# Optimization experiments

Measured on AMD Instinct MI355X. Metric: run time of the kernel, lower is better.

## Reference

```python
import jax, jax.numpy as jnp
import numpy as np

B, S, E, H = 2, 2048, 1024, 16
D = E // H  # head_dim = 64


def setup_inputs() -> dict:
    key = jax.random.key(0)
    ks = jax.random.split(key, 12)
    sc = 1.0 / np.sqrt(E)
    inp = {
        "query": jax.random.normal(ks[0], (B, S, E), jnp.float32),
        "key": jax.random.normal(ks[1], (B, S, E), jnp.float32),
        "value": jax.random.normal(ks[2], (B, S, E), jnp.float32),
        # causal mask: 1 where attending is allowed, 0 where blocked
        "mask": jnp.tril(jnp.ones((S, S), jnp.int32))[None, None, :, :],
        "Wq": jax.random.normal(ks[3], (E, E), jnp.float32) * sc,
        "bq": jax.random.normal(ks[4], (E,), jnp.float32) * sc,
        "Wk": jax.random.normal(ks[5], (E, E), jnp.float32) * sc,
        "bk": jax.random.normal(ks[6], (E,), jnp.float32) * sc,
        "Wv": jax.random.normal(ks[7], (E, E), jnp.float32) * sc,
        "bv": jax.random.normal(ks[8], (E,), jnp.float32) * sc,
        "Wo": jax.random.normal(ks[9], (E, E), jnp.float32) * sc,
        "bo": jax.random.normal(ks[10], (E,), jnp.float32) * sc,
    }
    return inp


def reference(query, key, value, mask, Wq, bq, Wk, bk, Wv, bv, Wo, bo):
    scale = jnp.asarray(np.sqrt(D), query.dtype)
    # Linear projections (torch Linear: x @ W.T + b)
    Q = query @ Wq.T + bq
    K = key @ Wk.T + bk
    V = value @ Wv.T + bv
    # [B, S, E] -> [B, H, S, D]
    Q = Q.reshape(B, -1, H, D).transpose(0, 2, 1, 3)
    K = K.reshape(B, -1, H, D).transpose(0, 2, 1, 3)
    V = V.reshape(B, -1, H, D).transpose(0, 2, 1, 3)
    # full [B, H, Sq, Sk] score matrix, as in the source
    scores = jnp.einsum("bhqd,bhkd->bhqk", Q, K) / scale
    scores = jnp.where(mask == 0, jnp.asarray(-1e10, scores.dtype), scores)
    weights = jax.nn.softmax(scores, axis=-1)
    weighted = jnp.einsum("bhqk,bhkd->bhqd", weights, V)
    concat = weighted.transpose(0, 2, 1, 3).reshape(B, -1, E)
    return concat @ Wo.T + bo
```

## Files before the change

### kernel.cpp

```cpp
#include <hip/hip_runtime.h>
#include <math.h>

#define BB 2
#define SS 2048
#define EE 1024
#define HH 16
#define DD 64

typedef unsigned short u16;
typedef __attribute__((ext_vector_type(8))) short short8;
typedef __attribute__((ext_vector_type(4))) float f32x4;

__device__ __forceinline__ u16 f2bf(float x) {
    union { float f; unsigned u; } v; v.f = x;
    return (u16)((v.u + 0x7fffu + ((v.u >> 16) & 1u)) >> 16);
}

__device__ __forceinline__ float exp2_fast(float x) {
    float r;
    asm("v_exp_f32 %0, %1" : "=v"(r) : "v"(x));
    return r;
}

#define GLL16(gp, lp) \
    __builtin_amdgcn_global_load_lds( \
        (const __attribute__((address_space(1))) void*)(gp), \
        (__attribute__((address_space(3))) void*)(lp), 16, 0, 0)

#define BARRIER do { asm volatile("" ::: "memory"); \
                     __builtin_amdgcn_s_barrier();  \
                     asm volatile("" ::: "memory"); } while (0)
#define VMW4 asm volatile("s_waitcnt vmcnt(4)" ::: "memory")
#define VMW0 asm volatile("s_waitcnt vmcnt(0)" ::: "memory")
#define LG0  asm volatile("s_waitcnt lgkmcnt(0)" ::: "memory")
#define SCHED0 __builtin_amdgcn_sched_barrier(0)

#define QSCALE 0.18033688f

__global__ __launch_bounds__(256)
void cvt_bf16(const float* __restrict__ s0, const float* __restrict__ s1,
              const float* __restrict__ s2, const float* __restrict__ s3,
              u16* __restrict__ d0, u16* __restrict__ d1,
              u16* __restrict__ d2, u16* __restrict__ d3)
{
    const int z = blockIdx.y;
    const float* s; u16* d;
    switch (z) {
        case 0: s = s0; d = d0; break;
        case 1: s = s1; d = d1; break;
        case 2: s = s2; d = d2; break;
        default: s = s3; d = d3; break;
    }
    const int i = (blockIdx.x * 256 + threadIdx.x) * 8;
    float4 a = *(const float4*)(s + i);
    float4 b = *(const float4*)(s + i + 4);
    short8 r;
    r[0] = (short)f2bf(a.x); r[1] = (short)f2bf(a.y);
    r[2] = (short)f2bf(a.z); r[3] = (short)f2bf(a.w);
    r[4] = (short)f2bf(b.x); r[5] = (short)f2bf(b.y);
    r[6] = (short)f2bf(b.z); r[7] = (short)f2bf(b.w);
    *(short8*)(d + i) = r;
}

__global__ __launch_bounds__(256, 3)
void gemm_qkv(const float* __restrict__ Xq, const float* __restrict__ Xk,
              const float* __restrict__ Xv,
              const u16* __restrict__ Wqb, const u16* __restrict__ Wkb,
              const u16* __restrict__ Wvb,
              const float* __restrict__ bq, const float* __restrict__ bk,
              const float* __restrict__ bv,
              u16* __restrict__ Qh, u16* __restrict__ Kh, u16* __restrict__ Vth)
{
    __shared__ __align__(16) u16 LS[2][2][128][32];
#define LA (LS[0])
#define LB (LS[1])

    const int bid = blockIdx.x;
    const int swz = (bid & 7) * 96 + (bid >> 3);
    const int z   = swz >> 8;
    const int rem = swz & 255;
    const int m0  = (rem >> 3) * 128;
    const int n0  = (rem & 7) * 128;

    const float* X = (z == 0) ? Xq : (z == 1) ? Xk : Xv;
    const u16* Wt = (z == 0) ? Wqb : (z == 1) ? Wkb : Wvb;
    const float* bias = (z == 0) ? bq : (z == 1) ? bk : bv;
    u16* out = (z == 0) ? Qh : (z == 1) ? Kh : Vth;

    const int t = threadIdx.x;
    const int w = t >> 6, l = t & 63;
    const int ln = l & 15, hi = l >> 4;
    const int wr = w >> 1, wc = w & 1;

    const int ar = t >> 1, ah = t & 1;
    const float* Xrow = X + (size_t)(m0 + ar) * 1024 + ah * 16;
    const int fa   = (ar >> 1) & 3;
    const int gpa0 = (2 * ah)     ^ fa;
    const int gpa1 = (2 * ah + 1) ^ fa;

    const int brow = t >> 2, gp4 = t & 3;
    const int gl4  = gp4 ^ (brow & 3);
    const u16* Wp0 = Wt + (size_t)(n0 + brow) * 1024 + gl4 * 8;
    const u16* Wp1 = Wt + (size_t)(n0 + 64 + brow) * 1024 + gl4 * 8;

    f32x4 acc[4][4];
    #pragma unroll
    for (int i = 0; i < 4; i++)
        #pragma unroll
        for (int j = 0; j < 4; j++)
            acc[i][j] = (f32x4){0.f, 0.f, 0.f, 0.f};

    float4 e0, e1, e2, e3;
    float4 o0, o1, o2, o3;

#define ISSUE_B(buf, k0_) {                                                  \
        GLL16(Wp0 + (k0_), &LB[buf][brow][gp4 * 8]);                         \
        GLL16(Wp1 + (k0_), &LB[buf][brow + 64][gp4 * 8]);                    \
    }
#define LOAD_A(S0, S1, S2, S3, k0_) {                                        \
        S0 = *(const float4*)(Xrow + (k0_));                                 \
        S1 = *(const float4*)(Xrow + (k0_) + 4);                             \
        S2 = *(const float4*)(Xrow + (k0_) + 8);                             \
        S3 = *(const float4*)(Xrow + (k0_) + 12);                            \
    }
#define CVT_A(buf, S0, S1, S2, S3) {                                         \
        uint4 u0, u1;                                                        \
        u0.x = f2bf(S0.x) | ((unsigned)f2bf(S0.y) << 16);                    \
        u0.y = f2bf(S0.z) | ((unsigned)f2bf(S0.w) << 16);                    \
        u0.z = f2bf(S1.x) | ((unsigned)f2bf(S1.y) << 16);                    \
        u0.w = f2bf(S1.z) | ((unsigned)f2bf(S1.w) << 16);                    \
        u1.x = f2bf(S2.x) | ((unsigned)f2bf(S2.y) << 16);                    \
        u1.y = f2bf(S2.z) | ((unsigned)f2bf(S2.w) << 16);                    \
        u1.z = f2bf(S3.x) | ((unsigned)f2bf(S3.y) << 16);                    \
        u1.w = f2bf(S3.z) | ((unsigned)f2bf(S3.w) << 16);                    \
        *(uint4*)&LA[buf][ar][gpa0 * 8] = u0;                                \
        *(uint4*)&LA[buf][ar][gpa1 * 8] = u1;                                \
    }
#define COMPUTE(la_, lb_) {                                                  \
        _Pragma("unroll")                                                    \
        for (int mi = 0; mi < 4; mi++)                                       \
            af[mi] = *(const short8*)&LA[la_][wr*64 + mi*16 + ln]            \
                         [(hi ^ ((ln >> 1) & 3)) * 8];                       \
        _Pragma("unroll")                                                    \
        for (int nj = 0; nj < 4; nj++)                                       \
            bf[nj] = *(const short8*)&LB[lb_][wc*64 + nj*16 + ln]            \
                         [(hi ^ (ln & 3)) * 8];                              \
        _Pragma("unroll")                                                    \
        for (int mi = 0; mi < 4; mi++)                                       \
            _Pragma("unroll")                                                \
            for (int nj = 0; nj < 4; nj++)                                   \
                acc[mi][nj] = __builtin_amdgcn_mfma_f32_16x16x32_bf16(       \
                    af[mi], bf[nj], acc[mi][nj], 0, 0, 0);                   \
    }

    short8 af[4], bf[4];

    LOAD_A(e0, e1, e2, e3, 0);
    CVT_A(0, e0, e1, e2, e3);
    ISSUE_B(0, 0); SCHED0;
    LOAD_A(o0, o1, o2, o3, 32); SCHED0;
    VMW4;
    LG0; BARRIER;

    for (int it = 0; it < 15; ++it) {
        const int k0 = it * 64;
        ISSUE_B(1, k0 + 32); SCHED0;
        LOAD_A(e0, e1, e2, e3, k0 + 64); SCHED0;
        COMPUTE(0, 0);
        CVT_A(1, o0, o1, o2, o3);
        VMW4;
        LG0; BARRIER;
        ISSUE_B(0, k0 + 64); SCHED0;
        LOAD_A(o0, o1, o2, o3, k0 + 96); SCHED0;
        COMPUTE(1, 1);
        CVT_A(0, e0, e1, e2, e3);
        VMW4;
        LG0; BARRIER;
    }
    ISSUE_B(1, 992); SCHED0;
    COMPUTE(0, 0);
    CVT_A(1, o0, o1, o2, o3);
    VMW0;
    LG0; BARRIER;
    COMPUTE(1, 1);
#undef ISSUE_B
#undef LOAD_A
#undef CVT_A
#undef COMPUTE

    u16* T = &LS[0][0][0][0];
    const int b = m0 >> 11;

    if (z == 2) {
        #pragma unroll
        for (int mi = 0; mi < 4; mi++) {
            #pragma unroll
            for (int nj = 0; nj < 4; nj++) {
                const int nc = wc * 64 + nj * 16 + ln;
                const float bv2 = bias[n0 + nc];
                const int sr0 = wr * 64 + mi * 16 + hi * 4;
                uint2 pk;
                pk.x = f2bf(acc[mi][nj][0] + bv2)
                     | ((unsigned)f2bf(acc[mi][nj][1] + bv2) << 16);
                pk.y = f2bf(acc[mi][nj][2] + bv2)
                     | ((unsigned)f2bf(acc[mi][nj][3] + bv2) << 16);
                const int gp = (sr0 >> 2) ^ (nc & 31);
                *(uint2*)&T[nc * 128 + gp * 4] = pk;
            }
        }
        __syncthreads();
        const int s0 = m0 & 2047;
        const int sidx = t & 15;
        const int ncr0 = t >> 4;
        #pragma unroll
        for (int i = 0; i < 8; i++) {
            const int nc = ncr0 + i * 16;
            const int a  = sidx * 2;
            const int pa = a ^ (nc & 31);
            const int pb = (a + 1) ^ (nc & 31);
            uint2 lo  = *(const uint2*)&T[nc * 128 + pa * 4];
            uint2 hi2 = *(const uint2*)&T[nc * 128 + pb * 4];
            uint4 vd = make_uint4(lo.x, lo.y, hi2.x, hi2.y);
            const int h = (n0 >> 6) + (nc >> 6);
            const int d = nc & 63;
            *(uint4*)&out[(((size_t)(b * HH + h) * 64 + d) << 11) + s0 + sidx * 8] = vd;
        }
    } else {
        #pragma unroll
        for (int mi = 0; mi < 4; mi++) {
            #pragma unroll
            for (int nj = 0; nj < 4; nj++) {
                const int nb = n0 + wc * 64 + nj * 16 + ln;
                const float bv2 = bias[nb];
                const int h = nb >> 6, d = nb & 63;
                #pragma unroll
                for (int r = 0; r < 4; r++) {
                    const int m = m0 + wr * 64 + mi * 16 + hi * 4 + r;
                    float v = acc[mi][nj][r] + bv2;
                    if (z == 0) v *= QSCALE;
                    const int s = m & 2047;
                    out[((((size_t)(b * HH + h)) << 11) + s) * 64 + d] = f2bf(v);
                }
            }
        }
    }
#undef LA
#undef LB
}

__global__ __launch_bounds__(256)
void gemm_out(const u16* __restrict__ Xb, const u16* __restrict__ Wb,
              const float* __restrict__ bias, float* __restrict__ outp)
{
    __shared__ __align__(16) u16 As[2][64][32];
    __shared__ __align__(16) u16 Bs[2][128][32];

    const int bid = blockIdx.x;
    const int swz = (bid & 7) * 64 + (bid >> 3);
    const int m0  = (swz >> 3) * 64;
    const int n0  = (swz & 7) * 128;

    const int t = threadIdx.x;
    const int w = t >> 6, l = t & 63;
    const int ln = l & 15, hi = l >> 4;
    const int wr = w >> 1, wc = w & 1;

    const int row0 = t >> 2, gp4 = t & 3;
    const int gl4  = gp4 ^ (row0 & 3);

    f32x4 acc[2][4];
    #pragma unroll
    for (int i = 0; i < 2; i++)
        #pragma unroll
        for (int j = 0; j < 4; j++)
            acc[i][j] = (f32x4){0.f, 0.f, 0.f, 0.f};

#define OSTAGE(buf, k0_) { \
    GLL16(Xb + (size_t)(m0 + row0) * 1024 + (k0_) + gl4 * 8,        \
          &As[buf][row0][gp4 * 8]);                                  \
    GLL16(Wb + (size_t)(n0 + row0) * 1024 + (k0_) + gl4 * 8,        \
          &Bs[buf][row0][gp4 * 8]);                                  \
    GLL16(Wb + (size_t)(n0 + 64 + row0) * 1024 + (k0_) + gl4 * 8,   \
          &Bs[buf][row0 + 64][gp4 * 8]); }

    OSTAGE(0, 0);
    __syncthreads();
    int cur = 0;
    for (int k0 = 0; k0 < 1024; k0 += 32) {
        if (k0 + 32 < 1024) OSTAGE(cur ^ 1, k0 + 32);
        short8 af[2], bfr[4];
        #pragma unroll
        for (int mi = 0; mi < 2; mi++)
            af[mi] = *(const short8*)&As[cur][wr*32 + mi*16 + ln][(hi ^ (ln & 3))*8];
        #pragma unroll
        for (int nj = 0; nj < 4; nj++)
            bfr[nj] = *(const short8*)&Bs[cur][wc*64 + nj*16 + ln][(hi ^ (ln & 3))*8];
        #pragma unroll
        for (int mi = 0; mi < 2; mi++)
            #pragma unroll
            for (int nj = 0; nj < 4; nj++)
                acc[mi][nj] = __builtin_amdgcn_mfma_f32_16x16x32_bf16(
                    af[mi], bfr[nj], acc[mi][nj], 0, 0, 0);
        __syncthreads();
        cur ^= 1;
    }
#undef OSTAGE

    #pragma unroll
    for (int mi = 0; mi < 2; mi++) {
        #pragma unroll
        for (int nj = 0; nj < 4; nj++) {
            const int nb = n0 + wc * 64 + nj * 16 + ln;
            const float bv2 = bias[nb];
            #pragma unroll
            for (int r = 0; r < 4; r++) {
                const int m = m0 + wr * 32 + mi * 16 + hi * 4 + r;
                outp[(size_t)m * 1024 + nb] = acc[mi][nj][r] + bv2;
            }
        }
    }
}

__global__ __launch_bounds__(256)
void attn_mfma(const u16* __restrict__ Qh, const u16* __restrict__ Kh,
               const u16* __restrict__ Vt, u16* __restrict__ Cc)
{
    __shared__ __align__(16) u16 Ks[2][2][4][64][8];
    __shared__ __align__(16) u16 Vs[2][2][4][64][8];
    __shared__ __align__(16) u16 Ps[4][16][64];
    const int bh = blockIdx.x;
    const int y  = 31 - blockIdx.y;
    const int q0 = y * 64;
    const int t = threadIdx.x, w = t >> 6, l = t & 63;
    const int ln = l & 15, hi = l >> 4;
    const size_t base = (size_t)bh * SS * DD;
    const int qg = q0 + w * 16 + ln;

    short8 qf0, qf1;
    {
        const u16* qp = Qh + base + (size_t)qg * 64 + hi * 8;
        qf0 = *(const short8*)qp;
        qf1 = *(const short8*)(qp + 32);
    }
    f32x4 o[4];
    #pragma unroll
    for (int dj = 0; dj < 4; dj++) o[dj] = (f32x4){0.f, 0.f, 0.f, 0.f};
    float mrun = -INFINITY, lrun = 0.f;

#define STAGE(buf, key0_)                                                        \
    {                                                                            \
        _Pragma("unroll")                                                        \
        for (int i_ = 0; i_ < 4; i_++) {                                         \
            const int id_ = w + i_ * 4;                                          \
            if (id_ < 8) {                                                       \
                const int dc_ = id_ >> 2, kg_ = id_ & 3;                         \
                const u16* gp_ = Kh + base + (size_t)((key0_) + l) * 64          \
                                 + dc_ * 32 + kg_ * 8;                           \
                GLL16(gp_, &Ks[buf][dc_][kg_][0][0]);                            \
            } else {                                                             \
                const int kc_ = (id_ >> 2) & 1, kg_ = id_ & 3;                   \
                const u16* gp_ = Vt + base + (size_t)l * SS + (key0_)            \
                                 + kc_ * 32 + kg_ * 8;                           \
                GLL16(gp_, &Vs[buf][kc_][kg_][0][0]);                            \
            }                                                                    \
        }                                                                        \
    }

    STAGE(0, 0);
    __syncthreads();
    int cur = 0;
    const int nkt = y + 1;
    for (int kt = 0; kt < nkt; kt++) {
        const int key0 = kt * 64;
        if (kt + 1 < nkt) STAGE(cur ^ 1, key0 + 64);

        f32x4 st[4];
        __builtin_amdgcn_s_setprio(1);
        #pragma unroll
        for (int kt4 = 0; kt4 < 4; kt4++) {
            short8 ka = *(const short8*)&Ks[cur][0][hi][kt4 * 16 + ln][0];
            short8 kb = *(const short8*)&Ks[cur][1][hi][kt4 * 16 + ln][0];
            f32x4 zz = (f32x4){0.f, 0.f, 0.f, 0.f};
            zz = __builtin_amdgcn_mfma_f32_16x16x32_bf16(ka, qf0, zz, 0, 0, 0);
            zz = __builtin_amdgcn_mfma_f32_16x16x32_bf16(kb, qf1, zz, 0, 0, 0);
            st[kt4] = zz;
        }
        __builtin_amdgcn_s_setprio(0);
        if (kt == y) {
            #pragma unroll
            for (int kt4 = 0; kt4 < 4; kt4++)
                #pragma unroll
                for (int r = 0; r < 4; r++)
                    if (key0 + kt4 * 16 + hi * 4 + r > qg)
                        st[kt4][r] = -INFINITY;
        }

        float tmax = -INFINITY;
        #pragma unroll
        for (int kt4 = 0; kt4 < 4; kt4++)
            #pragma unroll
            for (int r = 0; r < 4; r++)
                tmax = fmaxf(tmax, st[kt4][r]);
        tmax = fmaxf(tmax, __shfl_xor(tmax, 16));
        tmax = fmaxf(tmax, __shfl_xor(tmax, 32));
        if (__ballot(tmax > mrun + 8.f)) {
            const float mnew = fmaxf(mrun, tmax);
            const float alpha = exp2_fast(mrun - mnew);
            lrun *= alpha;
            mrun = mnew;
            #pragma unroll
            for (int r = 0; r < 4; r++) {
                const float ar = __shfl(alpha, hi * 4 + r);
                #pragma unroll
                for (int dj = 0; dj < 4; dj++) o[dj][r] *= ar;
            }
        }
        float p[4][4];
        float lsum = 0.f;
        #pragma unroll
        for (int kt4 = 0; kt4 < 4; kt4++)
            #pragma unroll
            for (int r = 0; r < 4; r++) {
                p[kt4][r] = exp2_fast(st[kt4][r] - mrun);
                lsum += p[kt4][r];
            }
        lsum += __shfl_xor(lsum, 16);
        lsum += __shfl_xor(lsum, 32);
        lrun += lsum;

        char* prow = ((char*)Ps) + (w * 16 + ln) * 128 + (hi & 1) * 8;
        #pragma unroll
        for (int kt4 = 0; kt4 < 4; kt4++) {
            unsigned dw0, dw1;
            asm("v_cvt_pk_bf16_f32 %0, %1, %2" : "=v"(dw0)
                : "v"(p[kt4][0]), "v"(p[kt4][1]));
            asm("v_cvt_pk_bf16_f32 %0, %1, %2" : "=v"(dw1)
                : "v"(p[kt4][2]), "v"(p[kt4][3]));
            const int g = (2 * kt4 + (hi >> 1)) ^ (ln & 7);
            *(uint2*)(prow + g * 16) = make_uint2(dw0, dw1);
        }

        __builtin_amdgcn_s_setprio(1);
        #pragma unroll
        for (int kc = 0; kc < 2; kc++) {
            const int gr = (kc * 4 + hi) ^ (ln & 7);
            short8 pa = *(const short8*)(((char*)Ps) + (w * 16 + ln) * 128 + gr * 16);
            #pragma unroll
            for (int dj = 0; dj < 4; dj++) {
                short8 vb = *(const short8*)&Vs[cur][kc][hi][dj * 16 + ln][0];
                o[dj] = __builtin_amdgcn_mfma_f32_16x16x32_bf16(pa, vb, o[dj], 0, 0, 0);
            }
        }
        __builtin_amdgcn_s_setprio(0);
        __syncthreads();
        cur ^= 1;
    }
#undef STAGE

    const float inv = 1.f / lrun;
    #pragma unroll
    for (int r = 0; r < 4; r++) {
        const float ir = __shfl(inv, hi * 4 + r);
        const int s = q0 + w * 16 + hi * 4 + r;
        const size_t ob = ((size_t)(bh >> 4) * SS + s) * EE + (bh & 15) * 64;
        #pragma unroll
        for (int dj = 0; dj < 4; dj++)
            Cc[ob + dj * 16 + ln] = f2bf(o[dj][r] * ir);
    }
}

extern "C" void kernel_launch(void* const* d_in, const int* in_sizes, int n_in,
                              void* d_out, int out_size, void* d_ws, size_t ws_size,
                              hipStream_t stream)
{
    (void)in_sizes; (void)n_in; (void)out_size; (void)ws_size;
    const float* query = (const float*)d_in[0];
    const float* key   = (const float*)d_in[1];
    const float* value = (const float*)d_in[2];
    const float* Wq = (const float*)d_in[4];
    const float* bq = (const float*)d_in[5];
    const float* Wk = (const float*)d_in[6];
    const float* bk = (const float*)d_in[7];
    const float* Wv = (const float*)d_in[8];
    const float* bv = (const float*)d_in[9];
    const float* Wo = (const float*)d_in[10];
    const float* bo = (const float*)d_in[11];
    float* out = (float*)d_out;

    char* ws = (char*)d_ws;
    u16* Wqb = (u16*)(ws + 25165824);
    u16* Wkb = (u16*)(ws + 27262976);
    u16* Wvb = (u16*)(ws + 29360128);
    u16* Wob = (u16*)(ws + 31457280);
    u16* Qh  = (u16*)(ws + 33554432);
    u16* Kh  = (u16*)(ws + 41943040);
    u16* Vth = (u16*)(ws + 50331648);
    u16* Cc  = (u16*)(ws + 58720256);

    cvt_bf16<<<dim3(512, 4), 256, 0, stream>>>(
        Wq, Wk, Wv, Wo, Wqb, Wkb, Wvb, Wob);

    gemm_qkv<<<768, 256, 0, stream>>>(
        query, key, value, Wqb, Wkb, Wvb, bq, bk, bv, Qh, Kh, Vth);
    attn_mfma<<<dim3(32, 32), 256, 0, stream>>>(Qh, Kh, Vth, Cc);
    gemm_out<<<512, 256, 0, stream>>>(Cc, Wob, bo, out);
}
```

Baseline: 117.5 us.

## Shrink QKV GEMM tile to 128x64 and double grid size for occupancy

Changes the QKV projection GEMM from 128x128 to 128x64 output tiles, with each wave owning 32 rows by 64 columns. The grid doubles to 1536 blocks, shared memory per block drops, and launch bounds rise to 4 blocks per CU. This is meant to fill all CUs and hide latency better. The cost is lower arithmetic intensity: the fp32 activation tile is loaded and converted to bf16 twice as often across the N dimension, and each block does less MFMA work per load.

```diff
diff --git a/kernel.cpp b/kernel.cpp
--- a/kernel.cpp
+++ b/kernel.cpp
@@ -62,7 +62,7 @@
     *(short8*)(d + i) = r;
 }
 
-__global__ __launch_bounds__(256, 3)
+__global__ __launch_bounds__(256, 4)
 void gemm_qkv(const float* __restrict__ Xq, const float* __restrict__ Xk,
               const float* __restrict__ Xv,
               const u16* __restrict__ Wqb, const u16* __restrict__ Wkb,
@@ -71,16 +71,18 @@
               const float* __restrict__ bv,
               u16* __restrict__ Qh, u16* __restrict__ Kh, u16* __restrict__ Vth)
 {
-    __shared__ __align__(16) u16 LS[2][2][128][32];
-#define LA (LS[0])
-#define LB (LS[1])
+    __shared__ __align__(16) u16 LS[12288];
+    typedef u16 rowA_t[128][32];
+    typedef u16 rowB_t[64][32];
+    rowA_t* LA = (rowA_t*)&LS[0];
+    rowB_t* LB = (rowB_t*)&LS[8192];
 
     const int bid = blockIdx.x;
-    const int swz = (bid & 7) * 96 + (bid >> 3);
-    const int z   = swz >> 8;
-    const int rem = swz & 255;
-    const int m0  = (rem >> 3) * 128;
-    const int n0  = (rem & 7) * 128;
+    const int swz = (bid & 7) * 192 + (bid >> 3);
+    const int z   = swz >> 9;
+    const int rem = swz & 511;
+    const int m0  = (rem >> 4) * 128;
+    const int n0  = (rem & 15) * 64;
 
     const float* X = (z == 0) ? Xq : (z == 1) ? Xk : Xv;
     const u16* Wt = (z == 0) ? Wqb : (z == 1) ? Wkb : Wvb;
@@ -90,7 +92,6 @@
     const int t = threadIdx.x;
     const int w = t >> 6, l = t & 63;
     const int ln = l & 15, hi = l >> 4;
-    const int wr = w >> 1, wc = w & 1;
 
     const int ar = t >> 1, ah = t & 1;
     const float* Xrow = X + (size_t)(m0 + ar) * 1024 + ah * 16;
@@ -101,11 +102,10 @@
     const int brow = t >> 2, gp4 = t & 3;
     const int gl4  = gp4 ^ (brow & 3);
     const u16* Wp0 = Wt + (size_t)(n0 + brow) * 1024 + gl4 * 8;
-    const u16* Wp1 = Wt + (size_t)(n0 + 64 + brow) * 1024 + gl4 * 8;
-
-    f32x4 acc[4][4];
+
+    f32x4 acc[2][4];
     #pragma unroll
-    for (int i = 0; i < 4; i++)
+    for (int i = 0; i < 2; i++)
         #pragma unroll
         for (int j = 0; j < 4; j++)
             acc[i][j] = (f32x4){0.f, 0.f, 0.f, 0.f};
@@ -115,7 +115,6 @@
 
 #define ISSUE_B(buf, k0_) {                                                  \
         GLL16(Wp0 + (k0_), &LB[buf][brow][gp4 * 8]);                         \
-        GLL16(Wp1 + (k0_), &LB[buf][brow + 64][gp4 * 8]);                    \
     }
 #define LOAD_A(S0, S1, S2, S3, k0_) {                                        \
         S0 = *(const float4*)(Xrow + (k0_));                                 \
@@ -138,22 +137,22 @@
     }
 #define COMPUTE(la_, lb_) {                                                  \
         _Pragma("unroll")                                                    \
-        for (int mi = 0; mi < 4; mi++)                                       \
-            af[mi] = *(const short8*)&LA[la_][wr*64 + mi*16 + ln]            \
+        for (int mi = 0; mi < 2; mi++)                                       \
+            af[mi] = *(const short8*)&LA[la_][w*32 + mi*16 + ln]             \
                          [(hi ^ ((ln >> 1) & 3)) * 8];                       \
         _Pragma("unroll")                                                    \
         for (int nj = 0; nj < 4; nj++)                                       \
-            bf[nj] = *(const short8*)&LB[lb_][wc*64 + nj*16 + ln]            \
+            bf[nj] = *(const short8*)&LB[lb_][nj*16 + ln]                    \
                          [(hi ^ (ln & 3)) * 8];                              \
         _Pragma("unroll")                                                    \
-        for (int mi = 0; mi < 4; mi++)                                       \
+        for (int mi = 0; mi < 2; mi++)                                       \
             _Pragma("unroll")                                                \
             for (int nj = 0; nj < 4; nj++)                                   \
                 acc[mi][nj] = __builtin_amdgcn_mfma_f32_16x16x32_bf16(       \
                     af[mi], bf[nj], acc[mi][nj], 0, 0, 0);                   \
     }
 
-    short8 af[4], bf[4];
+    short8 af[2], bf[4];
 
     LOAD_A(e0, e1, e2, e3, 0);
     CVT_A(0, e0, e1, e2, e3);
@@ -188,17 +187,18 @@
 #undef CVT_A
 #undef COMPUTE
 
-    u16* T = &LS[0][0][0][0];
+    u16* T = &LS[0];
     const int b = m0 >> 11;
+    const int h = n0 >> 6;
 
     if (z == 2) {
         #pragma unroll
-        for (int mi = 0; mi < 4; mi++) {
+        for (int mi = 0; mi < 2; mi++) {
             #pragma unroll
             for (int nj = 0; nj < 4; nj++) {
-                const int nc = wc * 64 + nj * 16 + ln;
+                const int nc = nj * 16 + ln;
                 const float bv2 = bias[n0 + nc];
-                const int sr0 = wr * 64 + mi * 16 + hi * 4;
+                const int sr0 = w * 32 + mi * 16 + hi * 4;
                 uint2 pk;
                 pk.x = f2bf(acc[mi][nj][0] + bv2)
                      | ((unsigned)f2bf(acc[mi][nj][1] + bv2) << 16);
@@ -213,7 +213,7 @@
         const int sidx = t & 15;
         const int ncr0 = t >> 4;
         #pragma unroll
-        for (int i = 0; i < 8; i++) {
+        for (int i = 0; i < 4; i++) {
             const int nc = ncr0 + i * 16;
             const int a  = sidx * 2;
             const int pa = a ^ (nc & 31);
@@ -221,21 +221,18 @@
             uint2 lo  = *(const uint2*)&T[nc * 128 + pa * 4];
             uint2 hi2 = *(const uint2*)&T[nc * 128 + pb * 4];
             uint4 vd = make_uint4(lo.x, lo.y, hi2.x, hi2.y);
-            const int h = (n0 >> 6) + (nc >> 6);
-            const int d = nc & 63;
-            *(uint4*)&out[(((size_t)(b * HH + h) * 64 + d) << 11) + s0 + sidx * 8] = vd;
+            *(uint4*)&out[(((size_t)(b * HH + h) * 64 + nc) << 11) + s0 + sidx * 8] = vd;
         }
     } else {
         #pragma unroll
-        for (int mi = 0; mi < 4; mi++) {
+        for (int mi = 0; mi < 2; mi++) {
             #pragma unroll
             for (int nj = 0; nj < 4; nj++) {
-                const int nb = n0 + wc * 64 + nj * 16 + ln;
-                const float bv2 = bias[nb];
-                const int h = nb >> 6, d = nb & 63;
+                const int d = nj * 16 + ln;
+                const float bv2 = bias[n0 + d];
                 #pragma unroll
                 for (int r = 0; r < 4; r++) {
-                    const int m = m0 + wr * 64 + mi * 16 + hi * 4 + r;
+                    const int m = m0 + w * 32 + mi * 16 + hi * 4 + r;
                     float v = acc[mi][nj][r] + bv2;
                     if (z == 0) v *= QSCALE;
                     const int s = m & 2047;
@@ -244,8 +241,6 @@
             }
         }
     }
-#undef LA
-#undef LB
 }
 
 __global__ __launch_bounds__(256)
@@ -500,7 +495,7 @@
     cvt_bf16<<<dim3(512, 4), 256, 0, stream>>>(
         Wq, Wk, Wv, Wo, Wqb, Wkb, Wvb, Wob);
 
-    gemm_qkv<<<768, 256, 0, stream>>>(
+    gemm_qkv<<<1536, 256, 0, stream>>>(
         query, key, value, Wqb, Wkb, Wvb, bq, bk, bv, Qh, Kh, Vth);
     attn_mfma<<<dim3(32, 32), 256, 0, stream>>>(Qh, Kh, Vth, Cc);
     gemm_out<<<512, 256, 0, stream>>>(Cc, Wob, bo, out);
```

Result: slower. 139.8 us (+18.9%).
